# Kernel optimization log

Measured on AMD Instinct MI355X. Metric: run time of the kernel, lower is better.

The kernel has to match this reference:

```python
import jax, jax.numpy as jnp
import numpy as np

N = 50_000        # nodes
D = 256           # emb_dim
L = 3             # num_layer
E = 4             # num_experts (all hop-1 GCN experts)
K = 2             # top-k gating
VOCAB = 5000      # src_vocab_size_graph
NEDGES = 1_600_000
BN_EPS = 1e-5


def setup_inputs() -> dict:
    key = jax.random.key(0)
    ks = jax.random.split(key, 8)
    x = jax.random.randint(ks[0], (N,), 0, VOCAB)                      # atom ids
    edge_index = jax.random.randint(ks[1], (2, NEDGES), 0, N)          # [2, E_edges] src/dst
    emb = jax.random.normal(ks[2], (VOCAB + 1, D), jnp.float32) * 0.02 # AtomEncoder table
    w_gate = jax.random.normal(ks[3], (L, D, E), jnp.float32) * 0.02   # per-layer gate
    conv_W = jax.random.normal(ks[4], (L, E, D, D), jnp.float32) * (1.0 / np.sqrt(D))
    conv_b = jnp.zeros((L, E, D), jnp.float32)
    bn_gamma = jnp.ones((L, E, D), jnp.float32)
    bn_beta = jnp.zeros((L, E, D), jnp.float32)
    return dict(x=x, edge_index=edge_index, emb=emb, w_gate=w_gate,
                conv_W=conv_W, conv_b=conv_b, bn_gamma=bn_gamma, bn_beta=bn_beta)


def reference(x, edge_index, emb, w_gate, conv_W, conv_b, bn_gamma, bn_beta):
    src, dst = edge_index[0], edge_index[1]
    ones = jnp.ones((NEDGES,), jnp.float32)
    out_deg = jax.ops.segment_sum(ones, src, num_segments=N)
    in_deg = jax.ops.segment_sum(ones, dst, num_segments=N)
    norm_src = jax.lax.rsqrt(jnp.maximum(out_deg, 1.0))[:, None]  # D^{-1/2} on source side
    norm_dst = jax.lax.rsqrt(jnp.maximum(in_deg, 1.0))[:, None]   # D^{-1/2} on dest side

    h = emb[x]  # [N, D] AtomEncoder
    node_ids = jnp.arange(N)[:, None]
    for l in range(L):
        # ---- top-k sparse gating over experts ----
        logits = h @ w_gate[l]                              # [N, E]
        topv, topi = jax.lax.top_k(logits, K)               # [N, K]
        gk = jax.nn.softmax(topv, axis=-1)                  # renormalized top-k gates
        gates = jnp.zeros((N, E), h.dtype).at[node_ids, topi].set(gk)  # sparse [N, E]
        # ---- shared symmetric-normalized GCN aggregation (same A_norm for all experts) ----
        msg = (h * norm_src)[src]                           # [E_edges, D]
        agg = jax.ops.segment_sum(msg, dst, num_segments=N) * norm_dst  # [N, D]
        # ---- per-expert linear + BatchNorm (training-mode stats over nodes) ----
        z = jnp.einsum('nd,edf->enf', agg, conv_W[l]) + conv_b[l][:, None, :]  # [E, N, D]
        mu = z.mean(axis=1, keepdims=True)
        var = z.var(axis=1, keepdims=True)
        z = (z - mu) * jax.lax.rsqrt(var + BN_EPS) * bn_gamma[l][:, None, :] + bn_beta[l][:, None, :]
        # ---- combine with sparse gates (zero gates => expert math cancels) ----
        h_moe = jnp.einsum('ne,enf->nf', gates, z)          # [N, D]
        # outer residual: h = h + drop_path(relu(h)); drop_path is identity in eval
        h = h_moe + jax.nn.relu(h_moe)
    return h  # JK='last' node representation [N, D]
```

## Files before the change

kernel.cpp:

```cpp
#include <hip/hip_runtime.h>
#include <hip/hip_bf16.h>

#define N_NODES 50000
#define DIM     256
#define NEXP    4
#define NLAYER  3
#define NEDGE   1600000
#define BN_EPS  1e-5f

typedef __attribute__((ext_vector_type(8))) short          s16x8;
typedef __attribute__((ext_vector_type(8))) unsigned short u16x8;
typedef __attribute__((ext_vector_type(4))) float          f32x4;

static __device__ __forceinline__ float wave_reduce(float v) {
    #pragma unroll
    for (int off = 32; off; off >>= 1) v += __shfl_xor(v, off, 64);
    return v;
}

static __device__ __forceinline__ void bf16split(float x, unsigned short& hi,
                                                 unsigned short& lo) {
    unsigned xb = __float_as_uint(x);
    unsigned hb = (xb + 0x7FFFu + ((xb >> 16) & 1u)) & 0xFFFF0000u;
    float hif = __uint_as_float(hb);
    float l  = x - hif;
    unsigned lb2 = __float_as_uint(l);
    unsigned lb  = (lb2 + 0x7FFFu + ((lb2 >> 16) & 1u)) >> 16;
    hi = (unsigned short)(hb >> 16);
    lo = (unsigned short)lb;
}

__global__ void k_deg(const int* __restrict__ src, const int* __restrict__ dst,
                      int* __restrict__ cnt_out, int* __restrict__ cnt_in) {
    int i = blockIdx.x * 256 + threadIdx.x;
    if (i < NEDGE) {
        atomicAdd(&cnt_out[src[i]], 1);
        atomicAdd(&cnt_in[dst[i]], 1);
    }
}

__global__ void k_norm(const int* __restrict__ cnt_out, const int* __restrict__ cnt_in,
                       float* __restrict__ nsrc, float* __restrict__ ndst) {
    int i = blockIdx.x * 256 + threadIdx.x;
    if (i < N_NODES) {
        nsrc[i] = rsqrtf(fmaxf((float)cnt_out[i], 1.f));
        ndst[i] = rsqrtf(fmaxf((float)cnt_in[i], 1.f));
    }
}

__global__ __launch_bounds__(1024) void k_scan(const int* __restrict__ cnt_in,
                                               int* __restrict__ offs,
                                               int* __restrict__ cursor) {
    __shared__ int ps[1024];
    const int CH = 49;
    int t = threadIdx.x;
    int base = t * CH;
    int s = 0;
    for (int k = 0; k < CH; k++) { int i = base + k; if (i < N_NODES) s += cnt_in[i]; }
    ps[t] = s; __syncthreads();
    for (int off = 1; off < 1024; off <<= 1) {
        int v = ps[t];
        int u = (t >= off) ? ps[t - off] : 0;
        __syncthreads();
        ps[t] = v + u;
        __syncthreads();
    }
    int run = (t == 0) ? 0 : ps[t - 1];
    for (int k = 0; k < CH; k++) {
        int i = base + k;
        if (i < N_NODES) { offs[i] = run; cursor[i] = run; run += cnt_in[i]; }
    }
    if (t == 1023) offs[N_NODES] = ps[1023];
}

__global__ void k_fill(const int* __restrict__ src, const int* __restrict__ dst,
                       int* __restrict__ cursor, int* __restrict__ csr_s) {
    int i = blockIdx.x * 256 + threadIdx.x;
    if (i < NEDGE) {
        int s = src[i], d = dst[i];
        int pos = atomicAdd(&cursor[d], 1);
        csr_s[pos] = s;
    }
}

__global__ void k_emb(const int* __restrict__ x, const float4* __restrict__ emb4,
                      float4* __restrict__ h4) {
    int i = blockIdx.x * 256 + threadIdx.x;
    if (i < N_NODES * 64) {
        int n = i >> 6, c = i & 63;
        h4[i] = emb4[x[n] * 64 + c];
    }
}

__global__ void k_gate(const float4* __restrict__ h4, const float4* __restrict__ wg4,
                       int* __restrict__ pid, float* __restrict__ gaN,
                       float* __restrict__ gbN) {
    int n    = blockIdx.x * 4 + (threadIdx.x >> 6);
    int lane = threadIdx.x & 63;
    if (n >= N_NODES) return;
    float4 hv = h4[n * 64 + lane];
    const float* hp = (const float*)&hv;
    float4 acc = {0.f, 0.f, 0.f, 0.f};
    #pragma unroll
    for (int j = 0; j < 4; j++) {
        float4 w = wg4[lane * 4 + j];
        acc.x += hp[j] * w.x; acc.y += hp[j] * w.y;
        acc.z += hp[j] * w.z; acc.w += hp[j] * w.w;
    }
    acc.x = wave_reduce(acc.x); acc.y = wave_reduce(acc.y);
    acc.z = wave_reduce(acc.z); acc.w = wave_reduce(acc.w);
    if (lane == 0) {
        float lg[4] = {acc.x, acc.y, acc.z, acc.w};
        int e1 = 0;
        #pragma unroll
        for (int e = 1; e < 4; e++) if (lg[e] > lg[e1]) e1 = e;
        int e2 = -1;
        #pragma unroll
        for (int e = 0; e < 4; e++) {
            if (e == e1) continue;
            if (e2 < 0 || lg[e] > lg[e2]) e2 = e;
        }
        float v1 = lg[e1], v2 = lg[e2];
        float g2 = 1.f / (1.f + expf(v1 - v2));
        float g1 = 1.f - g2;
        int a = min(e1, e2), b = max(e1, e2);
        float ga = (e1 < e2) ? g1 : g2;
        float gb = (e1 < e2) ? g2 : g1;
        int p = (a == 0) ? (b - 1) : ((a == 1) ? (b + 1) : (b + 2));
        pid[n] = p; gaN[n] = ga; gbN[n] = gb;
    }
}

__global__ void k_bucket(const int* __restrict__ pid,
                         int* __restrict__ gcount, int* __restrict__ bnode) {
    __shared__ int cnt[6];
    __shared__ int basep[6];
    int t = threadIdx.x;
    int n = blockIdx.x * 256 + t;
    if (t < 6) cnt[t] = 0;
    __syncthreads();
    int p = 0, pos = 0;
    bool valid = (n < N_NODES);
    if (valid) { p = pid[n]; pos = atomicAdd(&cnt[p], 1); }
    __syncthreads();
    if (t < 6) basep[t] = atomicAdd(&gcount[t], cnt[t]);
    __syncthreads();
    if (valid) bnode[p * N_NODES + basep[p] + pos] = n;
}

__global__ void k_agg(const float4* __restrict__ h4,
                      const int* __restrict__ offs,
                      const int* __restrict__ csr_s, const float* __restrict__ nsrc,
                      const float* __restrict__ ndst,
                      float4* __restrict__ agg4) {
    const float S  = 4294967296.0f;
    const float SI = 1.0f / 4294967296.0f;
    int n    = blockIdx.x * 4 + (threadIdx.x >> 6);
    int lane = threadIdx.x & 63;
    if (n >= N_NODES) return;
    int beg = offs[n], end = offs[n + 1];
    long long ax = 0, ay = 0, az = 0, aw = 0;
    int j = beg;
    for (; j + 1 < end; j += 2) {
        int   s0 = csr_s[j],     s1 = csr_s[j + 1];
        float w0 = nsrc[s0] * S, w1 = nsrc[s1] * S;
        float4 a = h4[(size_t)s0 * 64 + lane];
        float4 b = h4[(size_t)s1 * 64 + lane];
        ax += (long long)(w0 * a.x) + (long long)(w1 * b.x);
        ay += (long long)(w0 * a.y) + (long long)(w1 * b.y);
        az += (long long)(w0 * a.z) + (long long)(w1 * b.z);
        aw += (long long)(w0 * a.w) + (long long)(w1 * b.w);
    }
    if (j < end) {
        int   s0 = csr_s[j];
        float w0 = nsrc[s0] * S;
        float4 a = h4[(size_t)s0 * 64 + lane];
        ax += (long long)(w0 * a.x); ay += (long long)(w0 * a.y);
        az += (long long)(w0 * a.z); aw += (long long)(w0 * a.w);
    }
    float nd = ndst[n] * SI;
    float4 o;
    o.x = nd * (float)ax; o.y = nd * (float)ay;
    o.z = nd * (float)az; o.w = nd * (float)aw;
    agg4[n * 64 + lane] = o;
}

__global__ void k_apack(const float* __restrict__ agg, unsigned short* __restrict__ Apk) {
    int i = blockIdx.x * 256 + threadIdx.x;
    if (i < N_NODES * DIM) {
        int n = i >> 8, k = i & 255;
        unsigned short hi, lo;
        bf16split(agg[i], hi, lo);
        Apk[(size_t)n * 512 + k]       = hi;
        Apk[(size_t)n * 512 + 256 + k] = lo;
    }
}

__global__ void k_colsum(const float* __restrict__ agg, float* __restrict__ msum_p) {
    int t = threadIdx.x;
    const int CH = 200;
    int n0 = blockIdx.x * CH;
    float s = 0.f;
    for (int r = 0; r < CH; r++) {
        int n = n0 + r;
        if (n < N_NODES) s += agg[n * DIM + t];
    }
    msum_p[blockIdx.x * 256 + t] = s;
}

__global__ void k_msumred(const float* __restrict__ msum_p, float* __restrict__ msum) {
    int t = threadIdx.x;
    float s = 0.f;
    for (int b = 0; b < 250; b++) s += msum_p[b * 256 + t];
    msum[t] = s;
}

#define GSL   48
#define GCH   1056
#define NPAIR 10
__global__ __launch_bounds__(256) void k_gram(const float* __restrict__ agg,
                                              float* __restrict__ Cp) {
    __shared__ float LA[16][64];
    __shared__ float LB[16][64];
    const int tiT[NPAIR] = {0,0,0,0,1,1,1,2,2,3};
    const int tjT[NPAIR] = {0,1,2,3,1,2,3,2,3,3};
    int t  = threadIdx.x;
    int sl = blockIdx.x;
    int pr = blockIdx.y;
    int ti = tiT[pr], tj = tjT[pr];
    int tx = t & 15, ty = t >> 4;
    float acc[4][4] = {};
    int nbase = sl * GCH;
    const float4* agg4 = (const float4*)agg;
    for (int s0 = 0; s0 < GCH; s0 += 16) {
        int r = ty;
        int n = nbase + s0 + r;
        float4 va = {0.f, 0.f, 0.f, 0.f}, vb = {0.f, 0.f, 0.f, 0.f};
        if (n < N_NODES) {
            va = agg4[n * 64 + ti * 16 + tx];
            vb = agg4[n * 64 + tj * 16 + tx];
        }
        __syncthreads();
        *(float4*)&LA[r][tx * 4] = va;
        *(float4*)&LB[r][tx * 4] = vb;
        __syncthreads();
        #pragma unroll
        for (int rr = 0; rr < 16; rr++) {
            float4 a = *(const float4*)&LA[rr][tx * 4];
            float4 b = *(const float4*)&LB[rr][ty * 4];
            const float* af = (const float*)&a;
            const float* bf = (const float*)&b;
            #pragma unroll
            for (int i = 0; i < 4; i++)
                #pragma unroll
                for (int j = 0; j < 4; j++)
                    acc[i][j] += af[i] * bf[j];
        }
    }
    float* Cb = Cp + ((size_t)(sl * NPAIR + pr)) * 4096;
    #pragma unroll
    for (int i = 0; i < 4; i++) {
        float4 v; v.x = acc[i][0]; v.y = acc[i][1]; v.z = acc[i][2]; v.w = acc[i][3];
        *(float4*)&Cb[(tx * 4 + i) * 64 + ty * 4] = v;
    }
}

__global__ void k_gred(const float* __restrict__ Cp, float* __restrict__ Cm) {
    int gid = blockIdx.x * 256 + threadIdx.x;
    int i = gid >> 8, j = gid & 255;
    int a = i >> 6, b = j >> 6, ii = i & 63, jj = j & 63;
    int ro = ii, co = jj;
    if (a > b) { int tmp = a; a = b; b = tmp; ro = jj; co = ii; }
    int pr = (a == 0) ? b : ((a == 1) ? 3 + b : ((a == 2) ? 5 + b : 6 + b));
    const float* p = Cp + (size_t)pr * 4096 + ro * 64 + co;
    float s = 0.f;
    #pragma unroll 8
    for (int sl = 0; sl < GSL; sl++) s += p[(size_t)sl * NPAIR * 4096];
    Cm[gid] = s;
}

__global__ __launch_bounds__(256) void k_stats(const float* __restrict__ C,
                                               const float* __restrict__ msum,
                                               const float* __restrict__ conv_W,
                                               const float* __restrict__ bn_gamma,
                                               const float* __restrict__ bn_beta,
                                               float* __restrict__ scaleb,
                                               float* __restrict__ shiftb, int l) {
    int e = blockIdx.x >> 8, f = blockIdx.x & 255;
    int t = threadIdx.x;
    __shared__ float wsh[256];
    __shared__ float red[256];
    const float* W = conv_W + (size_t)(l * NEXP + e) * DIM * DIM;
    wsh[t] = W[t * DIM + f];
    __syncthreads();
    float v = 0.f;
    #pragma unroll 8
    for (int d2 = 0; d2 < DIM; d2++) v += C[d2 * DIM + t] * wsh[d2];
    float a_t = msum[t] * (1.f / (float)N_NODES);
    float qp  = wsh[t] * v;
    float ap  = a_t * wsh[t];
    red[t] = qp; __syncthreads();
    for (int off = 128; off; off >>= 1) { if (t < off) red[t] += red[t + off]; __syncthreads(); }
    float q = red[0];
    red[t] = ap; __syncthreads();
    for (int off = 128; off; off >>= 1) { if (t < off) red[t] += red[t + off]; __syncthreads(); }
    if (t == 0) {
        float aw  = red[0];
        float var = q * (1.f / (float)N_NODES) - aw * aw;
        var = fmaxf(var, 0.f);
        float sg = bn_gamma[(l * NEXP + e) * DIM + f] * rsqrtf(var + BN_EPS);
        scaleb[e * DIM + f] = sg;
        shiftb[e * DIM + f] = bn_beta[(l * NEXP + e) * DIM + f] - aw * sg;
    }
}

__global__ void k_wscale(const float* __restrict__ conv_W, const float* __restrict__ scaleb,
                         unsigned short* __restrict__ Wpk, int l) {
    int i = blockIdx.x * 256 + threadIdx.x;
    if (i < NEXP * DIM * DIM) {
        int k = i & 255, f = (i >> 8) & 255, e = i >> 16;
        float w = conv_W[(size_t)(l * NEXP + e) * 65536 + (size_t)k * 256 + f]
                * scaleb[e * 256 + f];
        unsigned short hi, lo;
        bf16split(w, hi, lo);
        size_t base = (size_t)(e * 256 + f) * 512;
        Wpk[base + k]       = hi;
        Wpk[base + 256 + k] = lo;
    }
}

__global__ __launch_bounds__(256) void k_moe(const unsigned short* __restrict__ Apk,
                                             const unsigned short* __restrict__ Wpk,
                                             const float* __restrict__ shiftb,
                                             const int* __restrict__ gcount,
                                             const int* __restrict__ bnode,
                                             const float* __restrict__ gaN,
                                             const float* __restrict__ gbN,
                                             float* __restrict__ hout) {
    __shared__ short As2[64][40];
    __shared__ short Wt[256][40];
    __shared__ int   nds[64];
    __shared__ float gA[64], gB[64];
    __shared__ float shc[2][256];
    int p    = blockIdx.y;
    int cnt  = gcount[p];
    int base = blockIdx.x * 64;
    if (base >= cnt) return;
    const int eaT[6] = {0,0,0,1,1,2};
    const int ebT[6] = {1,2,3,2,3,3};
    int ea = eaT[p], eb = ebT[p];
    int t  = threadIdx.x;
    if (t < 64) {
        int idx = base + t;
        if (idx < cnt) {
            int n = bnode[p * N_NODES + idx];
            nds[t] = n; gA[t] = gaN[n]; gB[t] = gbN[n];
        } else { nds[t] = -1; gA[t] = 0.f; gB[t] = 0.f; }
    }
    if (t < 128) {
        int which = t >> 6, c = t & 63;
        int e = which ? eb : ea;
        ((float4*)shc[which])[c] = ((const float4*)(shiftb + e * DIM))[c];
    }
    __syncthreads();

    int rA   = t >> 2;
    int cA8  = (t & 3) * 8;
    int fsub = t >> 2;
    int wc8  = (t & 3) * 8;

    int nrow = nds[rA];
    const unsigned short* arow = Apk + (size_t)(nrow < 0 ? 0 : nrow) * 512;

    u16x8 areg = {0,0,0,0,0,0,0,0};
    if (nrow >= 0) areg = *(const u16x8*)(arow + cA8);
    u16x8 wreg0, wreg1, wreg2, wreg3;
    {
        const unsigned short* wb = Wpk + (size_t)(ea * 256) * 512 + wc8;
        wreg0 = *(const u16x8*)(wb + (size_t)(fsub)       * 512);
        wreg1 = *(const u16x8*)(wb + (size_t)(64  + fsub) * 512);
        wreg2 = *(const u16x8*)(wb + (size_t)(128 + fsub) * 512);
        wreg3 = *(const u16x8*)(wb + (size_t)(192 + fsub) * 512);
    }

    int wv = t >> 6, lane = t & 63, quad = lane >> 4, l16 = lane & 15;
    f32x4 acc[4][4];
    #pragma unroll
    for (int a = 0; a < 4; a++)
        #pragma unroll
        for (int b = 0; b < 4; b++) { f32x4 z = {0.f,0.f,0.f,0.f}; acc[a][b] = z; }

    for (int s = 0; s < 64; s++) {
        __syncthreads();
        *(u16x8*)&As2[rA][cA8] = areg;
        *(u16x8*)&Wt[fsub][wc8]       = wreg0;
        *(u16x8*)&Wt[64  + fsub][wc8] = wreg1;
        *(u16x8*)&Wt[128 + fsub][wc8] = wreg2;
        *(u16x8*)&Wt[192 + fsub][wc8] = wreg3;
        __syncthreads();
        if (s < 63) {
            int s1   = s + 1;
            int esel = s1 >> 5;
            int t2   = (s1 >> 3) & 3;
            int kc   = (s1 & 7) * 32;
            int aoff = (t2 >= 2 ? 256 : 0) + kc;
            int woff = ((t2 & 1) ? 256 : 0) + kc;
            u16x8 z8 = {0,0,0,0,0,0,0,0};
            areg = z8;
            if (nrow >= 0) areg = *(const u16x8*)(arow + aoff + cA8);
            const unsigned short* wb = Wpk + (size_t)((esel ? eb : ea) * 256) * 512
                                     + woff + wc8;
            wreg0 = *(const u16x8*)(wb + (size_t)(fsub)       * 512);
            wreg1 = *(const u16x8*)(wb + (size_t)(64  + fsub) * 512);
            wreg2 = *(const u16x8*)(wb + (size_t)(128 + fsub) * 512);
            wreg3 = *(const u16x8*)(wb + (size_t)(192 + fsub) * 512);
        }
        s16x8 af[4], bfr[4];
        #pragma unroll
        for (int rt = 0; rt < 4; rt++)
            af[rt] = *(const s16x8*)&As2[rt * 16 + l16][quad * 8];
        #pragma unroll
        for (int ct = 0; ct < 4; ct++)
            bfr[ct] = *(const s16x8*)&Wt[wv * 64 + ct * 16 + l16][quad * 8];
        #pragma unroll
        for (int rt = 0; rt < 4; rt++)
            #pragma unroll
            for (int ct = 0; ct < 4; ct++)
                acc[rt][ct] = __builtin_amdgcn_mfma_f32_16x16x32_bf16(
                                  af[rt], bfr[ct], acc[rt][ct], 0, 0, 0);
        if (s == 31) {
            #pragma unroll
            for (int rt = 0; rt < 4; rt++)
                #pragma unroll
                for (int r = 0; r < 4; r++) {
                    int row = rt * 16 + quad * 4 + r;
                    float ratio = gA[row] / fmaxf(gB[row], 1e-30f);
                    #pragma unroll
                    for (int ct = 0; ct < 4; ct++) acc[rt][ct][r] *= ratio;
                }
        }
    }

    #pragma unroll
    for (int rt = 0; rt < 4; rt++)
        #pragma unroll
        for (int r = 0; r < 4; r++) {
            int row = rt * 16 + quad * 4 + r;
            int n = nds[row];
            if (n < 0) continue;
            float gaL = gA[row];
            float gbL = fmaxf(gB[row], 1e-30f);
            #pragma unroll
            for (int ct = 0; ct < 4; ct++) {
                int col = wv * 64 + ct * 16 + l16;
                float v = gbL * acc[rt][ct][r] + gaL * shc[0][col] + gbL * shc[1][col];
                hout[(size_t)n * DIM + col] = v + fmaxf(v, 0.f);
            }
        }
}

extern "C" void kernel_launch(void* const* d_in, const int* in_sizes, int n_in,
                              void* d_out, int out_size, void* d_ws, size_t ws_size,
                              hipStream_t stream) {
    const int*   x        = (const int*)d_in[0];
    const int*   ei       = (const int*)d_in[1];
    const float* emb      = (const float*)d_in[2];
    const float* w_gate   = (const float*)d_in[3];
    const float* conv_W   = (const float*)d_in[4];
    const float* bn_gamma = (const float*)d_in[6];
    const float* bn_beta  = (const float*)d_in[7];
    float* out = (float*)d_out;

    const int* src = ei;
    const int* dst = ei + NEDGE;

    char* ws = (char*)d_ws;
    size_t off = 0;
    auto alloc = [&](size_t bytes) -> void* {
        void* p = ws + off;
        off += (bytes + 255) & ~(size_t)255;
        return p;
    };
    float*          h       = (float*)alloc((size_t)N_NODES * DIM * 4);
    float*          agg     = (float*)alloc((size_t)N_NODES * DIM * 4);
    unsigned short* Apk     = (unsigned short*)alloc((size_t)N_NODES * 512 * 2);
    int*            cnt_out = (int*)  alloc((size_t)N_NODES * 4);
    int*            cnt_in  = (int*)  alloc((size_t)N_NODES * 4);
    float*          nsrc    = (float*)alloc((size_t)N_NODES * 4);
    float*          ndst    = (float*)alloc((size_t)N_NODES * 4);
    int*            offs    = (int*)  alloc((size_t)(N_NODES + 1) * 4);
    int*            cursor  = (int*)  alloc((size_t)N_NODES * 4);
    int*            csr_s   = (int*)  alloc((size_t)NEDGE * 4);
    int*            pid     = (int*)  alloc((size_t)N_NODES * 4);
    float*          gaN     = (float*)alloc((size_t)N_NODES * 4);
    float*          gbN     = (float*)alloc((size_t)N_NODES * 4);
    int*            gcount  = (int*)  alloc(6 * 4);
    int*            bnode   = (int*)  alloc((size_t)6 * N_NODES * 4);
    float*          Cp      = (float*)alloc((size_t)GSL * NPAIR * 4096 * 4);
    float*          Cm      = (float*)alloc((size_t)DIM * DIM * 4);
    float*          msum_p  = (float*)alloc((size_t)250 * 256 * 4);
    float*          msum    = (float*)alloc((size_t)DIM * 4);
    float*          scaleb  = (float*)alloc((size_t)NEXP * DIM * 4);
    float*          shiftb  = (float*)alloc((size_t)NEXP * DIM * 4);
    unsigned short* Wpk     = (unsigned short*)alloc((size_t)NEXP * DIM * 512 * 2);
    (void)ws_size; (void)in_sizes; (void)n_in; (void)out_size;

    hipMemsetAsync(cnt_out, 0, (size_t)N_NODES * 4, stream);
    hipMemsetAsync(cnt_in,  0, (size_t)N_NODES * 4, stream);
    k_deg <<<(NEDGE + 255) / 256, 256, 0, stream>>>(src, dst, cnt_out, cnt_in);
    k_norm<<<(N_NODES + 255) / 256, 256, 0, stream>>>(cnt_out, cnt_in, nsrc, ndst);
    k_scan<<<1, 1024, 0, stream>>>(cnt_in, offs, cursor);
    k_fill<<<(NEDGE + 255) / 256, 256, 0, stream>>>(src, dst, cursor, csr_s);
    k_emb <<<(N_NODES * 64 + 255) / 256, 256, 0, stream>>>(x, (const float4*)emb, (float4*)h);

    for (int l = 0; l < NLAYER; l++) {
        float* hout = (l == NLAYER - 1) ? out : h;

        k_gate<<<N_NODES / 4, 256, 0, stream>>>((const float4*)h,
                (const float4*)(w_gate + (size_t)l * DIM * NEXP), pid, gaN, gbN);
        hipMemsetAsync(gcount, 0, 6 * 4, stream);
        k_bucket<<<(N_NODES + 255) / 256, 256, 0, stream>>>(pid, gcount, bnode);
        k_agg<<<N_NODES / 4, 256, 0, stream>>>((const float4*)h, offs, csr_s, nsrc,
                ndst, (float4*)agg);
        k_apack<<<(N_NODES * DIM + 255) / 256, 256, 0, stream>>>(agg, Apk);

        k_colsum<<<250, 256, 0, stream>>>(agg, msum_p);
        k_msumred<<<1, 256, 0, stream>>>(msum_p, msum);
        k_gram<<<dim3(GSL, NPAIR), 256, 0, stream>>>(agg, Cp);
        k_gred<<<DIM * DIM / 256, 256, 0, stream>>>(Cp, Cm);
        k_stats<<<NEXP * DIM, 256, 0, stream>>>(Cm, msum, conv_W, bn_gamma, bn_beta,
                                                scaleb, shiftb, l);
        k_wscale<<<(NEXP * DIM * DIM + 255) / 256, 256, 0, stream>>>(conv_W, scaleb, Wpk, l);

        k_moe<<<dim3((N_NODES + 63) / 64, 6), 256, 0, stream>>>(Apk, Wpk, shiftb,
                gcount, bnode, gaN, gbN, hout);
    }
}
```

Baseline: 2.047 ms.

## Restructure GCN aggregation into column-sliced blocks with edge-parallel lanes

The aggregation kernel is rewritten so each block covers 8 nodes and one 16-column slice of a 128-column half, using a 2D grid. Within a wave, four lane groups each take a different edge, gather one float per lane, and combine partial sums with shuffles. Deterministic int64 fixed-point accumulation is replaced by truncated products summed in double, and csr loads and agg stores use nontemporal hints. Each node's edge list and norm lookups are now repeated for every column slice, and gathers become scalar 64-byte segments instead of full 1 KB rows, which trades memory-level parallelism against coalescing and redundant index reads.

```diff
diff --git a/kernel.cpp b/kernel.cpp
--- a/kernel.cpp
+++ b/kernel.cpp
@@ -148,41 +148,41 @@
     if (valid) bnode[p * N_NODES + basep[p] + pos] = n;
 }
 
-__global__ void k_agg(const float4* __restrict__ h4,
-                      const int* __restrict__ offs,
-                      const int* __restrict__ csr_s, const float* __restrict__ nsrc,
-                      const float* __restrict__ ndst,
-                      float4* __restrict__ agg4) {
+__global__ __launch_bounds__(512) void k_agg(const float* __restrict__ h,
+                                             const int* __restrict__ offs,
+                                             const int* __restrict__ csr_s,
+                                             const float* __restrict__ nsrc,
+                                             const float* __restrict__ ndst,
+                                             float* __restrict__ agg) {
     const float S  = 4294967296.0f;
     const float SI = 1.0f / 4294967296.0f;
-    int n    = blockIdx.x * 4 + (threadIdx.x >> 6);
-    int lane = threadIdx.x & 63;
-    if (n >= N_NODES) return;
+    int slice = blockIdx.x & 7;
+    int chunk = blockIdx.x >> 3;
+    int tid   = threadIdx.x;
+    int n     = chunk * 8 + (tid >> 6);
+    int lane  = tid & 63;
+    int g     = lane >> 4;
+    int col   = blockIdx.y * 128 + slice * 16 + (lane & 15);
     int beg = offs[n], end = offs[n + 1];
-    long long ax = 0, ay = 0, az = 0, aw = 0;
-    int j = beg;
-    for (; j + 1 < end; j += 2) {
-        int   s0 = csr_s[j],     s1 = csr_s[j + 1];
-        float w0 = nsrc[s0] * S, w1 = nsrc[s1] * S;
-        float4 a = h4[(size_t)s0 * 64 + lane];
-        float4 b = h4[(size_t)s1 * 64 + lane];
-        ax += (long long)(w0 * a.x) + (long long)(w1 * b.x);
-        ay += (long long)(w0 * a.y) + (long long)(w1 * b.y);
-        az += (long long)(w0 * a.z) + (long long)(w1 * b.z);
-        aw += (long long)(w0 * a.w) + (long long)(w1 * b.w);
-    }
-    if (j < end) {
-        int   s0 = csr_s[j];
-        float w0 = nsrc[s0] * S;
-        float4 a = h4[(size_t)s0 * 64 + lane];
-        ax += (long long)(w0 * a.x); ay += (long long)(w0 * a.y);
-        az += (long long)(w0 * a.z); aw += (long long)(w0 * a.w);
-    }
-    float nd = ndst[n] * SI;
-    float4 o;
-    o.x = nd * (float)ax; o.y = nd * (float)ay;
-    o.z = nd * (float)az; o.w = nd * (float)aw;
-    agg4[n * 64 + lane] = o;
+    double acc = 0.0;
+    #pragma unroll 4
+    for (int j = beg; j < end; j += 4) {
+        int eidx = j + g;
+        float w = 0.f, hv = 0.f;
+        if (eidx < end) {
+            int s = __builtin_nontemporal_load(&csr_s[eidx]);
+            w  = nsrc[s] * S;
+            hv = h[(size_t)s * 256 + col];
+        }
+        acc += (double)truncf(w * hv);
+    }
+    acc += __shfl_xor(acc, 16, 64);
+    acc += __shfl_xor(acc, 32, 64);
+    if (g == 0) {
+        float nd = ndst[n] * SI;
+        float o  = nd * (float)acc;
+        __builtin_nontemporal_store(o, &agg[(size_t)n * 256 + col]);
+    }
 }
 
 __global__ void k_apack(const float* __restrict__ agg, unsigned short* __restrict__ Apk) {
@@ -520,8 +520,7 @@
                 (const float4*)(w_gate + (size_t)l * DIM * NEXP), pid, gaN, gbN);
         hipMemsetAsync(gcount, 0, 6 * 4, stream);
         k_bucket<<<(N_NODES + 255) / 256, 256, 0, stream>>>(pid, gcount, bnode);
-        k_agg<<<N_NODES / 4, 256, 0, stream>>>((const float4*)h, offs, csr_s, nsrc,
-                ndst, (float4*)agg);
+        k_agg<<<dim3(6250 * 8, 2), 512, 0, stream>>>(h, offs, csr_s, nsrc, ndst, agg);
         k_apack<<<(N_NODES * DIM + 255) / 256, 256, 0, stream>>>(agg, Apk);
 
         k_colsum<<<250, 256, 0, stream>>>(agg, msum_p);
```

Result: slower. 4.234 ms (+106.8%).
